# Optimization experiments

Measured on AMD Instinct MI355X. Metric: run time of the kernel, lower is better.

Reference implementation:

```python
import jax, jax.numpy as jnp
import numpy as np
import math

RES = 600
RADIUS = 50.0
S, H, W = 8, 544, 960
N = RES * RES
HID = 64


def setup_inputs() -> dict:
    key = jax.random.key(0)
    ks = jax.random.split(key, 8)
    # fibonacci_sphere exactly as in the source (note: y = i/(N-1) - 1)
    i = np.arange(N, dtype=np.float64)
    phi = math.pi * (3.0 - math.sqrt(5.0))
    y = i / float(N - 1) - 1.0
    r = np.sqrt(np.clip(1.0 - y * y, 0.0, None))
    th = phi * i
    xyz = np.stack([np.cos(th) * r, y, np.sin(th) * r], axis=-1) * RADIUS
    bg_pcd = jnp.asarray(xyz.astype(np.float32))  # [N,3], center = 0
    # bg_scales = log(mean 3-NN distance); approximated analytically by the
    # mean point spacing on the sphere (values only; structure identical)
    d = RADIUS * math.sqrt(4.0 * math.pi / N)
    bg_scales = jnp.full((N, 3), math.log(d), dtype=jnp.float32)
    images = jax.random.normal(ks[0], (1, S, 3, H, W), dtype=jnp.float32)
    # viewmats: identity rotation + small translation jitter (valid poses)
    extrinsics = jnp.tile(jnp.eye(4, dtype=jnp.float32), (S, 1, 1))
    extrinsics = extrinsics.at[:, :3, 3].add(
        jax.random.normal(ks[1], (S, 3), dtype=jnp.float32) * 0.1)
    K = jnp.array([[500.0, 0.0, W / 2.0],
                   [0.0, 500.0, H / 2.0],
                   [0.0, 0.0, 1.0]], dtype=jnp.float32)
    intrinsics = jnp.tile(K, (S, 1, 1))
    # bg_field MLP params: Linear(3,64) -> ReLU -> Linear(64,6) -> Tanh
    W1 = jax.random.normal(ks[2], (3, HID), dtype=jnp.float32) / math.sqrt(3.0)
    b1 = jnp.zeros((HID,), dtype=jnp.float32)
    W2 = jax.random.normal(ks[3], (HID, 6), dtype=jnp.float32) / math.sqrt(HID)
    b2 = jnp.zeros((6,), dtype=jnp.float32)
    return {"images": images, "extrinsics": extrinsics, "intrinsics": intrinsics,
            "W1": W1, "b1": b1, "W2": W2, "b2": b2,
            "bg_pcd": bg_pcd, "bg_scales": bg_scales, "downsample": 1}


def _bilinear(img, px, py):
    # img: [3,H,W]; px,py: [N] pixel coords -> [N,3]
    Hh, Ww = img.shape[-2:]
    x0 = jnp.clip(jnp.floor(px), 0, Ww - 2).astype(jnp.int32)
    y0 = jnp.clip(jnp.floor(py), 0, Hh - 2).astype(jnp.int32)
    wx = px - x0
    wy = py - y0
    g = lambda yy, xx: img[:, yy, xx]  # [3,N]
    v = (g(y0, x0) * (1 - wx) * (1 - wy) + g(y0, x0 + 1) * wx * (1 - wy)
         + g(y0 + 1, x0) * (1 - wx) * wy + g(y0 + 1, x0 + 1) * wx * wy)
    return v.T  # [N,3]


def reference(images, extrinsics, intrinsics, W1, b1, W2, b2, bg_pcd, bg_scales, downsample):
    ds = jnp.float32(downsample)
    # scale_intrinsics: fx, fy, cx, cy divided by downsample
    D = jnp.array([[ds, 1.0, ds], [1.0, ds, ds], [1.0, 1.0, 1.0]], dtype=jnp.float32)
    Ks = intrinsics / D
    imgs = images[0]                      # [S,3,H,W]
    Hh, Ww = imgs.shape[-2:]
    xyz_h = jnp.concatenate([bg_pcd, jnp.ones_like(bg_pcd[:, :1])], axis=-1)  # [N,4]
    cam = jnp.einsum('sij,nj->sni', extrinsics[:, :3, :], xyz_h)  # [S,N,3]
    uv = jnp.einsum('sij,snj->sni', Ks, cam)                      # [S,N,3]
    z = uv[..., 2]
    zs = jnp.where(jnp.abs(z) > 1e-6, z, 1e-6)
    px = uv[..., 0] / zs
    py = uv[..., 1] / zs
    mask = (z > 1e-3) & (px >= 0) & (px <= Ww - 1) & (py >= 0) & (py <= Hh - 1)  # [S,N]
    feats = jax.vmap(_bilinear)(imgs, px, py)    # [S,N,3]
    m = mask.astype(feats.dtype)[..., None]
    cnt = jnp.maximum(m.sum(0), 1.0)
    feat = (feats * m).sum(0) / cnt              # [N,3] mean over visible views
    # bg_field: Linear -> ReLU -> Linear -> Tanh
    h = jax.nn.relu(feat @ W1 + b1)
    out6 = jnp.tanh(h @ W2 + b2)
    rgb = out6[:, :3]
    # background_scale_res is zeroed in the original, so scales = exp(bg_scales)
    scales = jnp.exp(bg_scales)
    proj_mask = mask.any(axis=0).astype(rgb.dtype)[:, None]
    return jnp.concatenate([rgb, scales], axis=-1) * proj_mask  # [N,6]
```

## Files before the change

### kernel.cpp

```cpp
#include <hip/hip_runtime.h>
#include <math.h>

#define NSV 8
#define NHID 64
#define IMG_H 544
#define IMG_W 960

__global__ __launch_bounds__(256) void sky_kernel(
    const float* __restrict__ images,
    const float* __restrict__ extr,
    const float* __restrict__ intr,
    const float* __restrict__ W1,
    const float* __restrict__ b1,
    const float* __restrict__ W2,
    const float* __restrict__ b2,
    const float* __restrict__ pcd,
    const float* __restrict__ lsc,
    const int*   __restrict__ dsp,
    float* __restrict__ out,
    int N)
{
    __shared__ float sE[NSV][12];
    __shared__ float sK[NSV][9];
    __shared__ float sW1[3][NHID];
    __shared__ float sB1[NHID];
    __shared__ float sW2[NHID][3];
    __shared__ float sB2[3];

    const int tid = threadIdx.x;

    if (tid < NSV) {
        const float ds = (float)dsp[0];
        const float* K = intr + tid * 9;
        const float* E = extr + tid * 16;
        sK[tid][0] = K[0] / ds; sK[tid][1] = K[1];      sK[tid][2] = K[2] / ds;
        sK[tid][3] = K[3];      sK[tid][4] = K[4] / ds; sK[tid][5] = K[5] / ds;
        sK[tid][6] = K[6];      sK[tid][7] = K[7];      sK[tid][8] = K[8];
        #pragma unroll
        for (int i = 0; i < 12; ++i) sE[tid][i] = E[i];
    }
    for (int i = tid; i < 3 * NHID; i += 256) sW1[i / NHID][i % NHID] = W1[i];
    if (tid < NHID) sB1[tid] = b1[tid];
    if (tid < NHID * 3) sW2[tid / 3][tid % 3] = W2[(tid / 3) * 6 + (tid % 3)];
    if (tid < 3) sB2[tid] = b2[tid];
    __syncthreads();

    const int n = blockIdx.x * 256 + tid;
    if (n >= N) return;

    const float x  = pcd[3 * n + 0];
    const float y  = pcd[3 * n + 1];
    const float zz = pcd[3 * n + 2];

    float f0 = 0.f, f1 = 0.f, f2 = 0.f;
    int cnt = 0;
    const int HW = IMG_H * IMG_W;

    #pragma unroll
    for (int s = 0; s < NSV; ++s) {
        const float cx = sE[s][0] * x + sE[s][1] * y + sE[s][2]  * zz + sE[s][3];
        const float cy = sE[s][4] * x + sE[s][5] * y + sE[s][6]  * zz + sE[s][7];
        const float cz = sE[s][8] * x + sE[s][9] * y + sE[s][10] * zz + sE[s][11];
        const float u = sK[s][0] * cx + sK[s][1] * cy + sK[s][2] * cz;
        const float v = sK[s][3] * cx + sK[s][4] * cy + sK[s][5] * cz;
        const float w = sK[s][6] * cx + sK[s][7] * cy + sK[s][8] * cz;
        const float zs = (fabsf(w) > 1e-6f) ? w : 1e-6f;
        const float px = u / zs;
        const float py = v / zs;
        const bool m = (w > 0.001f) && (px >= 0.f) && (px <= (float)(IMG_W - 1))
                                    && (py >= 0.f) && (py <= (float)(IMG_H - 1));
        if (m) {
            int x0 = (int)floorf(px); x0 = min(max(x0, 0), IMG_W - 2);
            int y0 = (int)floorf(py); y0 = min(max(y0, 0), IMG_H - 2);
            const float wx = px - (float)x0;
            const float wy = py - (float)y0;
            const float w00 = (1.f - wx) * (1.f - wy);
            const float w01 = wx * (1.f - wy);
            const float w10 = (1.f - wx) * wy;
            const float w11 = wx * wy;
            const float* p = images + (size_t)s * 3 * HW + (size_t)y0 * IMG_W + x0;
            f0 += p[0] * w00 + p[1] * w01 + p[IMG_W] * w10 + p[IMG_W + 1] * w11;
            p += HW;
            f1 += p[0] * w00 + p[1] * w01 + p[IMG_W] * w10 + p[IMG_W + 1] * w11;
            p += HW;
            f2 += p[0] * w00 + p[1] * w01 + p[IMG_W] * w10 + p[IMG_W + 1] * w11;
            ++cnt;
        }
    }

    const float s0 = expf(lsc[3 * n + 0]);
    const float s1 = expf(lsc[3 * n + 1]);
    const float s2 = expf(lsc[3 * n + 2]);

    float o0 = 0.f, o1 = 0.f, o2 = 0.f, pm = 0.f;
    if (cnt > 0) {
        const float c = (float)cnt;
        f0 /= c; f1 /= c; f2 /= c;
        float a0 = sB2[0], a1 = sB2[1], a2 = sB2[2];
        #pragma unroll 8
        for (int j = 0; j < NHID; ++j) {
            float h = f0 * sW1[0][j] + f1 * sW1[1][j] + f2 * sW1[2][j] + sB1[j];
            h = fmaxf(h, 0.f);
            a0 += h * sW2[j][0];
            a1 += h * sW2[j][1];
            a2 += h * sW2[j][2];
        }
        o0 = tanhf(a0); o1 = tanhf(a1); o2 = tanhf(a2);
        pm = 1.f;
    }

    float* op = out + (size_t)n * 6;
    op[0] = o0;
    op[1] = o1;
    op[2] = o2;
    op[3] = s0 * pm;
    op[4] = s1 * pm;
    op[5] = s2 * pm;
}

extern "C" void kernel_launch(void* const* d_in, const int* in_sizes, int n_in,
                              void* d_out, int out_size, void* d_ws, size_t ws_size,
                              hipStream_t stream) {
    const float* images = (const float*)d_in[0];
    const float* extr   = (const float*)d_in[1];
    const float* intr   = (const float*)d_in[2];
    const float* W1     = (const float*)d_in[3];
    const float* b1     = (const float*)d_in[4];
    const float* W2     = (const float*)d_in[5];
    const float* b2     = (const float*)d_in[6];
    const float* pcd    = (const float*)d_in[7];
    const float* lsc    = (const float*)d_in[8];
    const int*   dsp    = (const int*)d_in[9];
    float* out = (float*)d_out;

    const int N = in_sizes[7] / 3;
    const int blocks = (N + 255) / 256;
    sky_kernel<<<blocks, 256, 0, stream>>>(images, extr, intr, W1, b1, W2, b2,
                                           pcd, lsc, dsp, out, N);
}
```

Measured before the change: 124.0 us.

## Permute point-to-thread mapping with stride to balance visible points across warps

Each thread now handles point (g*377) mod N instead of point g. Visible and invisible points along the Fibonacci sphere then mix within each wavefront, which is meant to spread the divergent bilinear sampling and MLP work more evenly. The projection pass stores pixel coordinates and a mask bitmask first. A wave-level any() skips the gather and MLP entirely when no lane sees any view, the exp of scales runs only for visible points, and stores become float2. The price is scattered, non-coalesced reads of pcd and lsc and scattered output writes, and the permutation is a bijection only if 377 is coprime with N.

```diff
diff --git a/kernel.cpp b/kernel.cpp
--- a/kernel.cpp
+++ b/kernel.cpp
@@ -5,6 +5,7 @@
 #define NHID 64
 #define IMG_H 544
 #define IMG_W 960
+#define STRIDE 377
 
 __global__ __launch_bounds__(256) void sky_kernel(
     const float* __restrict__ images,
@@ -45,17 +46,17 @@
     if (tid < 3) sB2[tid] = b2[tid];
     __syncthreads();
 
-    const int n = blockIdx.x * 256 + tid;
-    if (n >= N) return;
+    const int g = blockIdx.x * 256 + tid;
+    if (g >= N) return;
+
+    const int n = (int)(((long long)g * STRIDE) % (long long)N);
 
     const float x  = pcd[3 * n + 0];
     const float y  = pcd[3 * n + 1];
     const float zz = pcd[3 * n + 2];
 
-    float f0 = 0.f, f1 = 0.f, f2 = 0.f;
-    int cnt = 0;
-    const int HW = IMG_H * IMG_W;
-
+    float pxs[NSV], pys[NSV];
+    int maskbits = 0;
     #pragma unroll
     for (int s = 0; s < NSV; ++s) {
         const float cx = sE[s][0] * x + sE[s][1] * y + sE[s][2]  * zz + sE[s][3];
@@ -67,55 +68,65 @@
         const float zs = (fabsf(w) > 1e-6f) ? w : 1e-6f;
         const float px = u / zs;
         const float py = v / zs;
+        pxs[s] = px; pys[s] = py;
         const bool m = (w > 0.001f) && (px >= 0.f) && (px <= (float)(IMG_W - 1))
                                     && (py >= 0.f) && (py <= (float)(IMG_H - 1));
-        if (m) {
-            int x0 = (int)floorf(px); x0 = min(max(x0, 0), IMG_W - 2);
-            int y0 = (int)floorf(py); y0 = min(max(y0, 0), IMG_H - 2);
-            const float wx = px - (float)x0;
-            const float wy = py - (float)y0;
-            const float w00 = (1.f - wx) * (1.f - wy);
-            const float w01 = wx * (1.f - wy);
-            const float w10 = (1.f - wx) * wy;
-            const float w11 = wx * wy;
-            const float* p = images + (size_t)s * 3 * HW + (size_t)y0 * IMG_W + x0;
-            f0 += p[0] * w00 + p[1] * w01 + p[IMG_W] * w10 + p[IMG_W + 1] * w11;
-            p += HW;
-            f1 += p[0] * w00 + p[1] * w01 + p[IMG_W] * w10 + p[IMG_W + 1] * w11;
-            p += HW;
-            f2 += p[0] * w00 + p[1] * w01 + p[IMG_W] * w10 + p[IMG_W + 1] * w11;
-            ++cnt;
+        maskbits |= (m ? (1 << s) : 0);
+    }
+
+    float o0 = 0.f, o1 = 0.f, o2 = 0.f;
+    float so0 = 0.f, so1 = 0.f, so2 = 0.f;
+
+    if (__any(maskbits != 0)) {
+        float f0 = 0.f, f1 = 0.f, f2 = 0.f;
+        int cnt = 0;
+        const int HW = IMG_H * IMG_W;
+
+        #pragma unroll
+        for (int s = 0; s < NSV; ++s) {
+            if (maskbits & (1 << s)) {
+                const float px = pxs[s], py = pys[s];
+                int x0 = (int)floorf(px); x0 = min(max(x0, 0), IMG_W - 2);
+                int y0 = (int)floorf(py); y0 = min(max(y0, 0), IMG_H - 2);
+                const float wx = px - (float)x0;
+                const float wy = py - (float)y0;
+                const float w00 = (1.f - wx) * (1.f - wy);
+                const float w01 = wx * (1.f - wy);
+                const float w10 = (1.f - wx) * wy;
+                const float w11 = wx * wy;
+                const float* p = images + (size_t)s * 3 * HW + (size_t)y0 * IMG_W + x0;
+                f0 += p[0] * w00 + p[1] * w01 + p[IMG_W] * w10 + p[IMG_W + 1] * w11;
+                p += HW;
+                f1 += p[0] * w00 + p[1] * w01 + p[IMG_W] * w10 + p[IMG_W + 1] * w11;
+                p += HW;
+                f2 += p[0] * w00 + p[1] * w01 + p[IMG_W] * w10 + p[IMG_W + 1] * w11;
+                ++cnt;
+            }
+        }
+
+        if (cnt > 0) {
+            const float c = (float)cnt;
+            f0 /= c; f1 /= c; f2 /= c;
+            float a0 = sB2[0], a1 = sB2[1], a2 = sB2[2];
+            #pragma unroll 8
+            for (int j = 0; j < NHID; ++j) {
+                float h = f0 * sW1[0][j] + f1 * sW1[1][j] + f2 * sW1[2][j] + sB1[j];
+                h = fmaxf(h, 0.f);
+                a0 += h * sW2[j][0];
+                a1 += h * sW2[j][1];
+                a2 += h * sW2[j][2];
+            }
+            o0 = tanhf(a0); o1 = tanhf(a1); o2 = tanhf(a2);
+            so0 = expf(lsc[3 * n + 0]);
+            so1 = expf(lsc[3 * n + 1]);
+            so2 = expf(lsc[3 * n + 2]);
         }
     }
 
-    const float s0 = expf(lsc[3 * n + 0]);
-    const float s1 = expf(lsc[3 * n + 1]);
-    const float s2 = expf(lsc[3 * n + 2]);
-
-    float o0 = 0.f, o1 = 0.f, o2 = 0.f, pm = 0.f;
-    if (cnt > 0) {
-        const float c = (float)cnt;
-        f0 /= c; f1 /= c; f2 /= c;
-        float a0 = sB2[0], a1 = sB2[1], a2 = sB2[2];
-        #pragma unroll 8
-        for (int j = 0; j < NHID; ++j) {
-            float h = f0 * sW1[0][j] + f1 * sW1[1][j] + f2 * sW1[2][j] + sB1[j];
-            h = fmaxf(h, 0.f);
-            a0 += h * sW2[j][0];
-            a1 += h * sW2[j][1];
-            a2 += h * sW2[j][2];
-        }
-        o0 = tanhf(a0); o1 = tanhf(a1); o2 = tanhf(a2);
-        pm = 1.f;
-    }
-
-    float* op = out + (size_t)n * 6;
-    op[0] = o0;
-    op[1] = o1;
-    op[2] = o2;
-    op[3] = s0 * pm;
-    op[4] = s1 * pm;
-    op[5] = s2 * pm;
+    float2* op = (float2*)(out + (size_t)n * 6);
+    op[0] = make_float2(o0, o1);
+    op[1] = make_float2(o2, so0);
+    op[2] = make_float2(so1, so2);
 }
 
 extern "C" void kernel_launch(void* const* d_in, const int* in_sizes, int n_in,
```

Result: slower. 133.3 us (+7.6%).
